# Optimization experiments

Measured on AMD Instinct MI355X. Metric: run time of the kernel, lower is better.

## Reference

```python
import jax, jax.numpy as jnp
import numpy as np

D_MODEL = 1024
N_HEADS = 16
HEAD_DIM = D_MODEL // N_HEADS
BATCH = 2
SEQ = 2048


def setup_inputs() -> dict:
    key = jax.random.key(0)
    ks = jax.random.split(key, 9)
    s = 1.0 / np.sqrt(D_MODEL)
    inp = {
        "x": jax.random.normal(ks[0], (BATCH, SEQ, D_MODEL), dtype=jnp.float32),
        "Wq": jax.random.uniform(ks[1], (D_MODEL, D_MODEL), jnp.float32, -s, s),
        "bq": jax.random.uniform(ks[2], (D_MODEL,), jnp.float32, -s, s),
        "Wk": jax.random.uniform(ks[3], (D_MODEL, D_MODEL), jnp.float32, -s, s),
        "bk": jax.random.uniform(ks[4], (D_MODEL,), jnp.float32, -s, s),
        "Wv": jax.random.uniform(ks[5], (D_MODEL, D_MODEL), jnp.float32, -s, s),
        "bv": jax.random.uniform(ks[6], (D_MODEL,), jnp.float32, -s, s),
        "Wo": jax.random.uniform(ks[7], (D_MODEL, D_MODEL), jnp.float32, -s, s),
        "bo": jax.random.uniform(ks[8], (D_MODEL,), jnp.float32, -s, s),
    }
    return inp


def reference(x, Wq, bq, Wk, bk, Wv, bv, Wo, bo):
    B, S, _ = x.shape
    # projections -> [B, H, S, Dh]
    def proj(W, b):
        y = jnp.einsum('bsd,df->bsf', x, W) + b
        return y.reshape(B, S, N_HEADS, HEAD_DIM).transpose(0, 2, 1, 3)
    q = proj(Wq, bq)
    k = proj(Wk, bk)
    v = proj(Wv, bv)
    scores = jnp.einsum('bhqd,bhkd->bhqk', q, k) / jnp.sqrt(jnp.float32(HEAD_DIM))
    mask = jnp.tril(jnp.ones((S, S), dtype=bool))  # [S, S] causal mask
    scores = jnp.where(mask, scores, -jnp.inf)
    weights = jax.nn.softmax(scores, axis=-1)
    h = jnp.einsum('bhqk,bhkd->bhqd', weights, v)
    h = h.transpose(0, 2, 1, 3).reshape(B, S, N_HEADS * HEAD_DIM)
    return jnp.einsum('bsd,df->bsf', h, Wo) + bo
```

## Files before the change

### kernel.cpp

```cpp
#include <hip/hip_runtime.h>
#include <hip/hip_bf16.h>
#include <cmath>

#define D_MODEL 1024
#define NHEADS 16
#define HDIM 64
#define BATCH 2
#define SEQ 2048
#define MROWS (BATCH*SEQ)
#define KDIM 1024

typedef unsigned short ushort_t;
typedef unsigned int uint32;
typedef __attribute__((ext_vector_type(8))) short short8;
typedef __attribute__((ext_vector_type(4))) short short4b;
typedef __attribute__((ext_vector_type(4))) float floatx4;

#define QSCALE 0.1803368801111204f
#define EXP2F(x) __builtin_amdgcn_exp2f(x)

__device__ __forceinline__ ushort_t f2bf(float x) {
    union { float f; uint32 u; } v; v.f = x;
    uint32 r = v.u + 0x7FFFu + ((v.u >> 16) & 1u);
    return (ushort_t)(r >> 16);
}

__device__ __forceinline__ uint32 pkbf(float a, float b) {
    union { __hip_bfloat162 h2; uint32 u; } v;
    v.h2 = __float22bfloat162_rn(make_float2(a, b));
    return v.u;
}

__device__ __forceinline__ void glds16(const void* g, void* l) {
    __builtin_amdgcn_global_load_lds(
        (const __attribute__((address_space(1))) void*)g,
        (__attribute__((address_space(3))) void*)l, 16, 0, 0);
}

__global__ __launch_bounds__(256)
void cvt_all(const float* __restrict__ x, const float* __restrict__ W0,
             const float* __restrict__ W1, const float* __restrict__ W2,
             const float* __restrict__ W3, ushort_t* __restrict__ xb,
             ushort_t* __restrict__ WtQKV, ushort_t* __restrict__ WtO)
{
    const int z = blockIdx.z;
    if (z == 4) {
        size_t idx = ((size_t)blockIdx.y * 32 + blockIdx.x) * 256 + threadIdx.x;
        #pragma unroll
        for (int l = 0; l < 4; ++l) {
            size_t i = ((size_t)l * 262144 + idx) * 4;
            float4 v = *(const float4*)(x + i);
            uint2 o;
            o.x = pkbf(v.x, v.y);
            o.y = pkbf(v.z, v.w);
            *(uint2*)(xb + i) = o;
        }
        return;
    }
    __shared__ float tl[32][33];
    const float* W = (z == 0) ? W0 : (z == 1) ? W1 : (z == 2) ? W2 : W3;
    ushort_t* out = (z < 3) ? (WtQKV + (size_t)z * D_MODEL * KDIM) : WtO;
    const int k0 = blockIdx.x * 32, n0 = blockIdx.y * 32;
    const int tx = threadIdx.x & 31, ty = threadIdx.x >> 5;
    #pragma unroll
    for (int i = 0; i < 4; ++i)
        tl[ty + i * 8][tx] = W[(size_t)(k0 + ty + i * 8) * D_MODEL + n0 + tx];
    __syncthreads();
    #pragma unroll
    for (int i = 0; i < 4; ++i)
        out[(size_t)(n0 + ty + i * 8) * KDIM + k0 + tx] = f2bf(tl[tx][ty + i * 8]);
}

__global__ __launch_bounds__(128, 2)
void gemm_qkv(const ushort_t* __restrict__ A, const ushort_t* __restrict__ Bt,
              const float* __restrict__ b0, const float* __restrict__ b1,
              const float* __restrict__ b2, ushort_t* __restrict__ Qb,
              ushort_t* __restrict__ Kb, ushort_t* __restrict__ Vb)
{
    __shared__ ushort_t As[128 * 64];
    __shared__ ushort_t Bs[128 * 64];

    const int tid = threadIdx.x;
    const int w = tid >> 6, lane = tid & 63;
    const int quad = lane >> 4, col = lane & 15;
    const int m0 = blockIdx.y * 128, n0 = blockIdx.x * 128;

    floatx4 zero = {0.f, 0.f, 0.f, 0.f};
    floatx4 acc[4][8];
    #pragma unroll
    for (int i = 0; i < 4; ++i)
        #pragma unroll
        for (int j = 0; j < 8; ++j) acc[i][j] = zero;

    #pragma unroll 1
    for (int k0 = 0; k0 < KDIM; k0 += 64) {
        #pragma unroll
        for (int i = 0; i < 8; ++i) {
            int c = i * 128 + tid;
            int row = c >> 3;
            int kc = (c & 7) ^ (row & 7);
            glds16(A  + (size_t)(m0 + row) * KDIM + k0 + kc * 8, As + (i * 128 + w * 64) * 8);
            glds16(Bt + (size_t)(n0 + row) * KDIM + k0 + kc * 8, Bs + (i * 128 + w * 64) * 8);
        }
        __syncthreads();
        #pragma unroll
        for (int ks = 0; ks < 2; ++ks) {
            short8 af[4], bfr[8];
            const int kc = ks * 4 + quad;
            #pragma unroll
            for (int mt = 0; mt < 4; ++mt) {
                int r = w * 64 + mt * 16 + col;
                af[mt] = *(const short8*)(As + ((size_t)r * 8 + (kc ^ (r & 7))) * 8);
            }
            #pragma unroll
            for (int nt = 0; nt < 8; ++nt) {
                int r = nt * 16 + col;
                bfr[nt] = *(const short8*)(Bs + ((size_t)r * 8 + (kc ^ (r & 7))) * 8);
            }
            #pragma unroll
            for (int mt = 0; mt < 4; ++mt)
                #pragma unroll
                for (int nt = 0; nt < 8; ++nt)
                    acc[mt][nt] = __builtin_amdgcn_mfma_f32_16x16x32_bf16(
                        af[mt], bfr[nt], acc[mt][nt], 0, 0, 0);
        }
        __syncthreads();
    }

    const int which = n0 >> 10;
    const float* bp = (which == 0) ? b0 : (which == 1) ? b1 : b2;
    if (which < 2) {
        ushort_t* outp = (which == 0) ? Qb : Kb;
        const float scl = (which == 0) ? QSCALE : 1.0f;
        #pragma unroll
        for (int mt = 0; mt < 4; ++mt)
            #pragma unroll
            for (int nt = 0; nt < 8; ++nt) {
                int nn = (n0 + nt * 16 + col) & 1023;
                float bb = bp[nn];
                int h = nn >> 6, d = nn & 63;
                #pragma unroll
                for (int r = 0; r < 4; ++r) {
                    int m = m0 + w * 64 + mt * 16 + quad * 4 + r;
                    int b = m >> 11, s = m & 2047;
                    outp[((size_t)(b * NHEADS + h) * SEQ + s) * HDIM + d] =
                        f2bf((acc[mt][nt][r] + bb) * scl);
                }
            }
    } else {
        #pragma unroll
        for (int mt = 0; mt < 4; ++mt)
            #pragma unroll
            for (int nt = 0; nt < 8; ++nt) {
                int nn = (n0 + nt * 16 + col) & 1023;
                float bb = bp[nn];
                int h = nn >> 6, d = nn & 63;
                int mb = m0 + w * 64 + mt * 16 + quad * 4;
                int b = mb >> 11, s = mb & 2047;
                uint2 pw;
                pw.x = pkbf(acc[mt][nt][0] + bb, acc[mt][nt][1] + bb);
                pw.y = pkbf(acc[mt][nt][2] + bb, acc[mt][nt][3] + bb);
                *(uint2*)(Vb + ((size_t)(b * NHEADS + h) * HDIM + d) * SEQ + s) = pw;
            }
    }
}

__global__ __launch_bounds__(128, 2)
void gemm_o(const ushort_t* __restrict__ A, const ushort_t* __restrict__ Bt,
            const float* __restrict__ b0, float* __restrict__ Cf)
{
    __shared__ ushort_t As[128 * 64];
    __shared__ ushort_t Bs[64 * 64];

    const int tid = threadIdx.x;
    const int w = tid >> 6, lane = tid & 63;
    const int quad = lane >> 4, col = lane & 15;
    const int m0 = blockIdx.y * 128, n0 = blockIdx.x * 64;

    floatx4 zero = {0.f, 0.f, 0.f, 0.f};
    floatx4 acc[4][4];
    #pragma unroll
    for (int i = 0; i < 4; ++i)
        #pragma unroll
        for (int j = 0; j < 4; ++j) acc[i][j] = zero;

    #pragma unroll 1
    for (int k0 = 0; k0 < KDIM; k0 += 64) {
        #pragma unroll
        for (int i = 0; i < 8; ++i) {
            int c = i * 128 + tid;
            int row = c >> 3;
            int kc = (c & 7) ^ (row & 7);
            glds16(A + (size_t)(m0 + row) * KDIM + k0 + kc * 8, As + (i * 128 + w * 64) * 8);
        }
        #pragma unroll
        for (int i = 0; i < 4; ++i) {
            int c = i * 128 + tid;
            int row = c >> 3;
            int kc = (c & 7) ^ (row & 7);
            glds16(Bt + (size_t)(n0 + row) * KDIM + k0 + kc * 8, Bs + (i * 128 + w * 64) * 8);
        }
        __syncthreads();
        #pragma unroll
        for (int ks = 0; ks < 2; ++ks) {
            short8 af[4], bfr[4];
            const int kc = ks * 4 + quad;
            #pragma unroll
            for (int mt = 0; mt < 4; ++mt) {
                int r = w * 64 + mt * 16 + col;
                af[mt] = *(const short8*)(As + ((size_t)r * 8 + (kc ^ (r & 7))) * 8);
            }
            #pragma unroll
            for (int nt = 0; nt < 4; ++nt) {
                int r = nt * 16 + col;
                bfr[nt] = *(const short8*)(Bs + ((size_t)r * 8 + (kc ^ (r & 7))) * 8);
            }
            #pragma unroll
            for (int mt = 0; mt < 4; ++mt)
                #pragma unroll
                for (int nt = 0; nt < 4; ++nt)
                    acc[mt][nt] = __builtin_amdgcn_mfma_f32_16x16x32_bf16(
                        af[mt], bfr[nt], acc[mt][nt], 0, 0, 0);
        }
        __syncthreads();
    }

    #pragma unroll
    for (int mt = 0; mt < 4; ++mt)
        #pragma unroll
        for (int nt = 0; nt < 4; ++nt) {
            int n = n0 + nt * 16 + col;
            float bb = b0[n];
            #pragma unroll
            for (int r = 0; r < 4; ++r) {
                int m = m0 + w * 64 + mt * 16 + quad * 4 + r;
                Cf[(size_t)m * D_MODEL + n] = acc[mt][nt][r] + bb;
            }
        }
}

__global__ __launch_bounds__(256)
void attn_mfma(const ushort_t* __restrict__ Q, const ushort_t* __restrict__ K,
               const ushort_t* __restrict__ Vt, ushort_t* __restrict__ H)
{
    __shared__ __align__(16) float smemf[16640];
    ushort_t* Qs  = (ushort_t*)smemf;
    ushort_t* Ksm = (ushort_t*)(smemf + 2048);
    ushort_t* Vsm = (ushort_t*)(smemf + 6144);
    float* Ored = smemf;
    float* Lred = smemf + 16384;

    const int tid = threadIdx.x;
    const int w = tid >> 6, lane = tid & 63;
    const int quad = lane >> 4, col = lane & 15;
    const int blk = blockIdx.x;
    const int bh = (blk & 7) * 4 + ((blk >> 3) & 3);
    const int pair = blk >> 5;
    const size_t base = (size_t)bh * SEQ * HDIM;
    const ushort_t* Kb = K + base;
    const ushort_t* Vb = Vt + base;
    const int b = bh >> 4, h = bh & 15;

    const int c0 = (w * 2 + 0) * 64 + lane;
    const int c1 = (w * 2 + 1) * 64 + lane;
    const int r0 = c0 >> 3, o0 = ((c0 & 7) ^ (r0 & 7)) * 8;
    const int r1 = c1 >> 3, o1 = ((c1 & 7) ^ (r1 & 7)) * 8;

    const int rk = w * 16 + col;
    const floatx4 zero = {0.f, 0.f, 0.f, 0.f};

    #pragma unroll 1
    for (int pi = 0; pi < 2; ++pi) {
        const int qt = pi ? pair : 31 - pair;
        const int q0 = qt * 64;
        const int nt = qt + 1;

        __syncthreads();
        #pragma unroll
        for (int i = 0; i < 2; ++i) {
            int c = (w * 2 + i) * 64 + lane;
            int row = c >> 3, kc = (c & 7) ^ (row & 7);
            glds16(Q + base + (size_t)(q0 + row) * HDIM + kc * 8, Qs + (w * 2 + i) * 512);
        }
        glds16(Kb + (size_t)r0 * HDIM + o0, Ksm + (w * 2 + 0) * 512);
        glds16(Kb + (size_t)r1 * HDIM + o1, Ksm + (w * 2 + 1) * 512);
        glds16(Vb + (size_t)r0 * SEQ + o0,  Vsm + (w * 2 + 0) * 512);
        glds16(Vb + (size_t)r1 * SEQ + o1,  Vsm + (w * 2 + 1) * 512);
        __syncthreads();

        short8 bq[4][2];
        #pragma unroll
        for (int qb = 0; qb < 4; ++qb)
            #pragma unroll
            for (int ks = 0; ks < 2; ++ks) {
                int rq = qb * 16 + col;
                int kc = ks * 4 + quad;
                bq[qb][ks] = *(const short8*)(Qs + ((size_t)rq * 8 + (kc ^ (rq & 7))) * 8);
            }

        floatx4 o_[4][4];
        #pragma unroll
        for (int i = 0; i < 4; ++i)
            #pragma unroll
            for (int j = 0; j < 4; ++j) o_[i][j] = zero;
        float lq[4] = {0.f, 0.f, 0.f, 0.f};

        #pragma unroll 1
        for (int t = 0; t < nt; ++t) {
            const ushort_t* Kcur = Ksm + (t & 1) * 4096;
            const ushort_t* Vcur = Vsm + (t & 1) * 4096;
            if (t + 1 < nt) {
                const int k0n = (t + 1) * 64;
                ushort_t* Kn = Ksm + ((t + 1) & 1) * 4096;
                ushort_t* Vn = Vsm + ((t + 1) & 1) * 4096;
                glds16(Kb + (size_t)(k0n + r0) * HDIM + o0, Kn + (w * 2 + 0) * 512);
                glds16(Kb + (size_t)(k0n + r1) * HDIM + o1, Kn + (w * 2 + 1) * 512);
                glds16(Vb + (size_t)r0 * SEQ + k0n + o0,    Vn + (w * 2 + 0) * 512);
                glds16(Vb + (size_t)r1 * SEQ + k0n + o1,    Vn + (w * 2 + 1) * 512);
            }

            floatx4 sc[4];
            #pragma unroll
            for (int qb = 0; qb < 4; ++qb) sc[qb] = zero;
            #pragma unroll
            for (int ks = 0; ks < 2; ++ks) {
                const int kc = ks * 4 + quad;
                short8 ak = *(const short8*)(Kcur + ((size_t)rk * 8 + (kc ^ (rk & 7))) * 8);
                #pragma unroll
                for (int qb = 0; qb < 4; ++qb)
                    sc[qb] = __builtin_amdgcn_mfma_f32_16x16x32_bf16(
                        ak, bq[qb][ks], sc[qb], 0, 0, 0);
            }

            if (t == nt - 1) {
                #pragma unroll
                for (int qb = 0; qb < 4; ++qb)
                    #pragma unroll
                    for (int r = 0; r < 4; ++r)
                        if (w * 16 + quad * 4 + r > qb * 16 + col) sc[qb][r] = -INFINITY;
            }

            short4b bp[4];
            #pragma unroll
            for (int qb = 0; qb < 4; ++qb) {
                float p0 = EXP2F(sc[qb][0]);
                float p1 = EXP2F(sc[qb][1]);
                float p2 = EXP2F(sc[qb][2]);
                float p3 = EXP2F(sc[qb][3]);
                lq[qb] += (p0 + p1) + (p2 + p3);
                union { uint2 u; short4b s; } pv;
                pv.u.x = pkbf(p0, p1);
                pv.u.y = pkbf(p2, p3);
                bp[qb] = pv.s;
            }

            const int cc = 2 * w + (quad >> 1);
            const int sub = (quad & 1) * 4;
            #pragma unroll
            for (int db = 0; db < 4; ++db) {
                int rv = db * 16 + col;
                short4b av = *(const short4b*)(Vcur + ((size_t)rv * 8 + (cc ^ (rv & 7))) * 8 + sub);
                #pragma unroll
                for (int qb = 0; qb < 4; ++qb)
                    o_[db][qb] = __builtin_amdgcn_mfma_f32_16x16x16bf16_1k(
                        av, bp[qb], o_[db][qb], 0, 0, 0);
            }

            __syncthreads();
        }

        #pragma unroll
        for (int qb = 0; qb < 4; ++qb) {
            lq[qb] += __shfl_xor(lq[qb], 16);
            lq[qb] += __shfl_xor(lq[qb], 32);
        }
        if (quad == 0) {
            #pragma unroll
            for (int qb = 0; qb < 4; ++qb) Lred[w * 64 + qb * 16 + col] = lq[qb];
        }
        {
            float* myreg = Ored + w * 4096;
            #pragma unroll
            for (int db = 0; db < 4; ++db)
                #pragma unroll
                for (int qb = 0; qb < 4; ++qb) {
                    int q = qb * 16 + col;
                    int swch = (db * 4 + quad) ^ col;
                    *(floatx4*)(myreg + q * 64 + swch * 4) = o_[db][qb];
                }
        }
        __syncthreads();

        {
            const int qloc = w * 16 + (lane >> 2);
            float lsum = Lred[qloc] + Lred[64 + qloc] + Lred[128 + qloc] + Lred[192 + qloc];
            float linv = 1.f / lsum;
            const int dc0 = (lane & 3) * 4;
            floatx4 acc[4];
            #pragma unroll
            for (int j = 0; j < 4; ++j) {
                int swch = (dc0 + j) ^ (qloc & 15);
                const float* p = Ored + (size_t)qloc * 64 + swch * 4;
                floatx4 a = *(const floatx4*)p;
                a += *(const floatx4*)(p + 4096);
                a += *(const floatx4*)(p + 8192);
                a += *(const floatx4*)(p + 12288);
                acc[j] = a;
            }
            const size_t rowb = ((size_t)(b * SEQ + q0 + qloc)) * D_MODEL + h * HDIM + dc0 * 4;
            uint4 u0, u1;
            u0.x = pkbf(acc[0][0] * linv, acc[0][1] * linv);
            u0.y = pkbf(acc[0][2] * linv, acc[0][3] * linv);
            u0.z = pkbf(acc[1][0] * linv, acc[1][1] * linv);
            u0.w = pkbf(acc[1][2] * linv, acc[1][3] * linv);
            u1.x = pkbf(acc[2][0] * linv, acc[2][1] * linv);
            u1.y = pkbf(acc[2][2] * linv, acc[2][3] * linv);
            u1.z = pkbf(acc[3][0] * linv, acc[3][1] * linv);
            u1.w = pkbf(acc[3][2] * linv, acc[3][3] * linv);
            *(uint4*)(H + rowb) = u0;
            *(uint4*)(H + rowb + 8) = u1;
        }
    }
}

extern "C" void kernel_launch(void* const* d_in, const int* in_sizes, int n_in,
                              void* d_out, int out_size, void* d_ws, size_t ws_size,
                              hipStream_t stream)
{
    (void)in_sizes; (void)n_in; (void)out_size; (void)ws_size;
    const float* x  = (const float*)d_in[0];
    const float* Wq = (const float*)d_in[1];
    const float* bq = (const float*)d_in[2];
    const float* Wk = (const float*)d_in[3];
    const float* bk = (const float*)d_in[4];
    const float* Wv = (const float*)d_in[5];
    const float* bv = (const float*)d_in[6];
    const float* Wo = (const float*)d_in[7];
    const float* bo = (const float*)d_in[8];

    const size_t E = (size_t)MROWS * D_MODEL;
    ushort_t* xb    = (ushort_t*)d_ws;
    ushort_t* WtQKV = xb + E;
    ushort_t* WtO   = WtQKV + 3 * (size_t)D_MODEL * KDIM;
    ushort_t* Qb    = WtO + (size_t)D_MODEL * KDIM;
    ushort_t* Kb    = Qb + E;
    ushort_t* Vb    = Kb + E;
    ushort_t* Hb    = Vb + E;

    cvt_all<<<dim3(32, 32, 5), 256, 0, stream>>>(x, Wq, Wk, Wv, Wo, xb, WtQKV, WtO);
    gemm_qkv<<<dim3(24, 32), 128, 0, stream>>>(xb, WtQKV, bq, bk, bv, Qb, Kb, Vb);
    attn_mfma<<<dim3(512), 256, 0, stream>>>(Qb, Kb, Vb, Hb);
    gemm_o<<<dim3(16, 32), 128, 0, stream>>>(Hb, WtO, bo, (float*)d_out);
}
```

Baseline: 179.2 us.

## Split attention into one query tile per block, shrink LDS, add MFMA priority

The attention kernel now launches one block per query tile (1024 blocks) instead of pairing a long and a short tile in each block. The output reduction is done in two halves over head dimension, which cuts shared memory from about 65KB to 40KB, and launch bounds request 4 blocks per CU to raise occupancy. s_setprio is raised around the MFMA sections to favour matrix issue across waves. In exchange, the causal workload is less balanced per block and Q is loaded per tile, so scheduling now depends on the hardware dispatching heavy tiles first.

Result: slower. 367.9 us (+105.3%).

```diff
diff --git a/kernel.cpp b/kernel.cpp
--- a/kernel.cpp
+++ b/kernel.cpp
@@ -239,23 +239,25 @@
         }
 }
 
-__global__ __launch_bounds__(256)
+__global__ __launch_bounds__(256, 4)
 void attn_mfma(const ushort_t* __restrict__ Q, const ushort_t* __restrict__ K,
                const ushort_t* __restrict__ Vt, ushort_t* __restrict__ H)
 {
-    __shared__ __align__(16) float smemf[16640];
+    __shared__ __align__(16) float smemf[10240];
     ushort_t* Qs  = (ushort_t*)smemf;
     ushort_t* Ksm = (ushort_t*)(smemf + 2048);
     ushort_t* Vsm = (ushort_t*)(smemf + 6144);
-    float* Ored = smemf;
-    float* Lred = smemf + 16384;
+    float* Lred = smemf;
+    float* Ored = smemf + 2048;
 
     const int tid = threadIdx.x;
     const int w = tid >> 6, lane = tid & 63;
     const int quad = lane >> 4, col = lane & 15;
     const int blk = blockIdx.x;
-    const int bh = (blk & 7) * 4 + ((blk >> 3) & 3);
-    const int pair = blk >> 5;
+    const int g5 = blk & 31;
+    const int bh = (g5 & 7) * 4 + (g5 >> 3);
+    const int grp = blk >> 5;
+    const int qt = (grp < 16) ? (31 - 2 * grp) : (2 * (grp - 16));
     const size_t base = (size_t)bh * SEQ * HDIM;
     const ushort_t* Kb = K + base;
     const ushort_t* Vb = Vt + base;
@@ -269,157 +271,164 @@
     const int rk = w * 16 + col;
     const floatx4 zero = {0.f, 0.f, 0.f, 0.f};
 
+    const int q0 = qt * 64;
+    const int nt = qt + 1;
+
+    #pragma unroll
+    for (int i = 0; i < 2; ++i) {
+        int c = (w * 2 + i) * 64 + lane;
+        int row = c >> 3, kc = (c & 7) ^ (row & 7);
+        glds16(Q + base + (size_t)(q0 + row) * HDIM + kc * 8, Qs + (w * 2 + i) * 512);
+    }
+    glds16(Kb + (size_t)r0 * HDIM + o0, Ksm + (w * 2 + 0) * 512);
+    glds16(Kb + (size_t)r1 * HDIM + o1, Ksm + (w * 2 + 1) * 512);
+    glds16(Vb + (size_t)r0 * SEQ + o0,  Vsm + (w * 2 + 0) * 512);
+    glds16(Vb + (size_t)r1 * SEQ + o1,  Vsm + (w * 2 + 1) * 512);
+    __syncthreads();
+
+    short8 bq[4][2];
+    #pragma unroll
+    for (int qb = 0; qb < 4; ++qb)
+        #pragma unroll
+        for (int ks = 0; ks < 2; ++ks) {
+            int rq = qb * 16 + col;
+            int kc = ks * 4 + quad;
+            bq[qb][ks] = *(const short8*)(Qs + ((size_t)rq * 8 + (kc ^ (rq & 7))) * 8);
+        }
+
+    floatx4 o_[4][4];
+    #pragma unroll
+    for (int i = 0; i < 4; ++i)
+        #pragma unroll
+        for (int j = 0; j < 4; ++j) o_[i][j] = zero;
+    float lq[4] = {0.f, 0.f, 0.f, 0.f};
+
     #pragma unroll 1
-    for (int pi = 0; pi < 2; ++pi) {
-        const int qt = pi ? pair : 31 - pair;
-        const int q0 = qt * 64;
-        const int nt = qt + 1;
-
-        __syncthreads();
-        #pragma unroll
-        for (int i = 0; i < 2; ++i) {
-            int c = (w * 2 + i) * 64 + lane;
-            int row = c >> 3, kc = (c & 7) ^ (row & 7);
-            glds16(Q + base + (size_t)(q0 + row) * HDIM + kc * 8, Qs + (w * 2 + i) * 512);
-        }
-        glds16(Kb + (size_t)r0 * HDIM + o0, Ksm + (w * 2 + 0) * 512);
-        glds16(Kb + (size_t)r1 * HDIM + o1, Ksm + (w * 2 + 1) * 512);
-        glds16(Vb + (size_t)r0 * SEQ + o0,  Vsm + (w * 2 + 0) * 512);
-        glds16(Vb + (size_t)r1 * SEQ + o1,  Vsm + (w * 2 + 1) * 512);
-        __syncthreads();
-
-        short8 bq[4][2];
-        #pragma unroll
-        for (int qb = 0; qb < 4; ++qb)
-            #pragma unroll
-            for (int ks = 0; ks < 2; ++ks) {
-                int rq = qb * 16 + col;
-                int kc = ks * 4 + quad;
-                bq[qb][ks] = *(const short8*)(Qs + ((size_t)rq * 8 + (kc ^ (rq & 7))) * 8);
-            }
-
-        floatx4 o_[4][4];
-        #pragma unroll
-        for (int i = 0; i < 4; ++i)
-            #pragma unroll
-            for (int j = 0; j < 4; ++j) o_[i][j] = zero;
-        float lq[4] = {0.f, 0.f, 0.f, 0.f};
-
-        #pragma unroll 1
-        for (int t = 0; t < nt; ++t) {
-            const ushort_t* Kcur = Ksm + (t & 1) * 4096;
-            const ushort_t* Vcur = Vsm + (t & 1) * 4096;
-            if (t + 1 < nt) {
-                const int k0n = (t + 1) * 64;
-                ushort_t* Kn = Ksm + ((t + 1) & 1) * 4096;
-                ushort_t* Vn = Vsm + ((t + 1) & 1) * 4096;
-                glds16(Kb + (size_t)(k0n + r0) * HDIM + o0, Kn + (w * 2 + 0) * 512);
-                glds16(Kb + (size_t)(k0n + r1) * HDIM + o1, Kn + (w * 2 + 1) * 512);
-                glds16(Vb + (size_t)r0 * SEQ + k0n + o0,    Vn + (w * 2 + 0) * 512);
-                glds16(Vb + (size_t)r1 * SEQ + k0n + o1,    Vn + (w * 2 + 1) * 512);
-            }
-
-            floatx4 sc[4];
-            #pragma unroll
-            for (int qb = 0; qb < 4; ++qb) sc[qb] = zero;
-            #pragma unroll
-            for (int ks = 0; ks < 2; ++ks) {
-                const int kc = ks * 4 + quad;
-                short8 ak = *(const short8*)(Kcur + ((size_t)rk * 8 + (kc ^ (rk & 7))) * 8);
+    for (int t = 0; t < nt; ++t) {
+        const ushort_t* Kcur = Ksm + (t & 1) * 4096;
+        const ushort_t* Vcur = Vsm + (t & 1) * 4096;
+        if (t + 1 < nt) {
+            const int k0n = (t + 1) * 64;
+            ushort_t* Kn = Ksm + ((t + 1) & 1) * 4096;
+            ushort_t* Vn = Vsm + ((t + 1) & 1) * 4096;
+            glds16(Kb + (size_t)(k0n + r0) * HDIM + o0, Kn + (w * 2 + 0) * 512);
+            glds16(Kb + (size_t)(k0n + r1) * HDIM + o1, Kn + (w * 2 + 1) * 512);
+            glds16(Vb + (size_t)r0 * SEQ + k0n + o0,    Vn + (w * 2 + 0) * 512);
+            glds16(Vb + (size_t)r1 * SEQ + k0n + o1,    Vn + (w * 2 + 1) * 512);
+        }
+
+        floatx4 sc[4];
+        #pragma unroll
+        for (int qb = 0; qb < 4; ++qb) sc[qb] = zero;
+        __builtin_amdgcn_s_setprio(1);
+        #pragma unroll
+        for (int ks = 0; ks < 2; ++ks) {
+            const int kc = ks * 4 + quad;
+            short8 ak = *(const short8*)(Kcur + ((size_t)rk * 8 + (kc ^ (rk & 7))) * 8);
+            #pragma unroll
+            for (int qb = 0; qb < 4; ++qb)
+                sc[qb] = __builtin_amdgcn_mfma_f32_16x16x32_bf16(
+                    ak, bq[qb][ks], sc[qb], 0, 0, 0);
+        }
+        __builtin_amdgcn_s_setprio(0);
+
+        if (t == nt - 1) {
+            #pragma unroll
+            for (int qb = 0; qb < 4; ++qb)
                 #pragma unroll
-                for (int qb = 0; qb < 4; ++qb)
-                    sc[qb] = __builtin_amdgcn_mfma_f32_16x16x32_bf16(
-                        ak, bq[qb][ks], sc[qb], 0, 0, 0);
-            }
-
-            if (t == nt - 1) {
-                #pragma unroll
-                for (int qb = 0; qb < 4; ++qb)
-                    #pragma unroll
-                    for (int r = 0; r < 4; ++r)
-                        if (w * 16 + quad * 4 + r > qb * 16 + col) sc[qb][r] = -INFINITY;
-            }
-
-            short4b bp[4];
-            #pragma unroll
-            for (int qb = 0; qb < 4; ++qb) {
-                float p0 = EXP2F(sc[qb][0]);
-                float p1 = EXP2F(sc[qb][1]);
-                float p2 = EXP2F(sc[qb][2]);
-                float p3 = EXP2F(sc[qb][3]);
-                lq[qb] += (p0 + p1) + (p2 + p3);
-                union { uint2 u; short4b s; } pv;
-                pv.u.x = pkbf(p0, p1);
-                pv.u.y = pkbf(p2, p3);
-                bp[qb] = pv.s;
-            }
-
-            const int cc = 2 * w + (quad >> 1);
-            const int sub = (quad & 1) * 4;
-            #pragma unroll
-            for (int db = 0; db < 4; ++db) {
-                int rv = db * 16 + col;
-                short4b av = *(const short4b*)(Vcur + ((size_t)rv * 8 + (cc ^ (rv & 7))) * 8 + sub);
-                #pragma unroll
-                for (int qb = 0; qb < 4; ++qb)
-                    o_[db][qb] = __builtin_amdgcn_mfma_f32_16x16x16bf16_1k(
-                        av, bp[qb], o_[db][qb], 0, 0, 0);
-            }
-
-            __syncthreads();
-        }
-
+                for (int r = 0; r < 4; ++r)
+                    if (w * 16 + quad * 4 + r > qb * 16 + col) sc[qb][r] = -INFINITY;
+        }
+
+        short4b bp[4];
         #pragma unroll
         for (int qb = 0; qb < 4; ++qb) {
-            lq[qb] += __shfl_xor(lq[qb], 16);
-            lq[qb] += __shfl_xor(lq[qb], 32);
-        }
-        if (quad == 0) {
-            #pragma unroll
-            for (int qb = 0; qb < 4; ++qb) Lred[w * 64 + qb * 16 + col] = lq[qb];
-        }
+            float p0 = EXP2F(sc[qb][0]);
+            float p1 = EXP2F(sc[qb][1]);
+            float p2 = EXP2F(sc[qb][2]);
+            float p3 = EXP2F(sc[qb][3]);
+            lq[qb] += (p0 + p1) + (p2 + p3);
+            union { uint2 u; short4b s; } pv;
+            pv.u.x = pkbf(p0, p1);
+            pv.u.y = pkbf(p2, p3);
+            bp[qb] = pv.s;
+        }
+
+        const int cc = 2 * w + (quad >> 1);
+        const int sub = (quad & 1) * 4;
+        __builtin_amdgcn_s_setprio(1);
+        #pragma unroll
+        for (int db = 0; db < 4; ++db) {
+            int rv = db * 16 + col;
+            short4b av = *(const short4b*)(Vcur + ((size_t)rv * 8 + (cc ^ (rv & 7))) * 8 + sub);
+            #pragma unroll
+            for (int qb = 0; qb < 4; ++qb)
+                o_[db][qb] = __builtin_amdgcn_mfma_f32_16x16x16bf16_1k(
+                    av, bp[qb], o_[db][qb], 0, 0, 0);
+        }
+        __builtin_amdgcn_s_setprio(0);
+
+        __syncthreads();
+    }
+
+    #pragma unroll
+    for (int qb = 0; qb < 4; ++qb) {
+        lq[qb] += __shfl_xor(lq[qb], 16);
+        lq[qb] += __shfl_xor(lq[qb], 32);
+    }
+    if (quad == 0) {
+        #pragma unroll
+        for (int qb = 0; qb < 4; ++qb) Lred[w * 64 + qb * 16 + col] = lq[qb];
+    }
+
+    float linv = 0.f;
+    const int lr = lane >> 2;
+    const int qloc = w * 16 + lr;
+    const int dg = lane & 3;
+    #pragma unroll 1
+    for (int p = 0; p < 2; ++p) {
         {
-            float* myreg = Ored + w * 4096;
-            #pragma unroll
-            for (int db = 0; db < 4; ++db)
+            float* myreg = Ored + w * 2048;
+            #pragma unroll
+            for (int dh = 0; dh < 2; ++dh) {
                 #pragma unroll
                 for (int qb = 0; qb < 4; ++qb) {
                     int q = qb * 16 + col;
-                    int swch = (db * 4 + quad) ^ col;
-                    *(floatx4*)(myreg + q * 64 + swch * 4) = o_[db][qb];
+                    int dc = dh * 4 + quad;
+                    int swch = dc ^ (q & 7);
+                    *(floatx4*)(myreg + q * 32 + swch * 4) = o_[p * 2 + dh][qb];
                 }
-        }
-        __syncthreads();
-
+            }
+        }
+        __syncthreads();
         {
-            const int qloc = w * 16 + (lane >> 2);
-            float lsum = Lred[qloc] + Lred[64 + qloc] + Lred[128 + qloc] + Lred[192 + qloc];
-            float linv = 1.f / lsum;
-            const int dc0 = (lane & 3) * 4;
-            floatx4 acc[4];
-            #pragma unroll
-            for (int j = 0; j < 4; ++j) {
-                int swch = (dc0 + j) ^ (qloc & 15);
-                const float* p = Ored + (size_t)qloc * 64 + swch * 4;
-                floatx4 a = *(const floatx4*)p;
-                a += *(const floatx4*)(p + 4096);
-                a += *(const floatx4*)(p + 8192);
-                a += *(const floatx4*)(p + 12288);
-                acc[j] = a;
-            }
-            const size_t rowb = ((size_t)(b * SEQ + q0 + qloc)) * D_MODEL + h * HDIM + dc0 * 4;
-            uint4 u0, u1;
-            u0.x = pkbf(acc[0][0] * linv, acc[0][1] * linv);
-            u0.y = pkbf(acc[0][2] * linv, acc[0][3] * linv);
-            u0.z = pkbf(acc[1][0] * linv, acc[1][1] * linv);
-            u0.w = pkbf(acc[1][2] * linv, acc[1][3] * linv);
-            u1.x = pkbf(acc[2][0] * linv, acc[2][1] * linv);
-            u1.y = pkbf(acc[2][2] * linv, acc[2][3] * linv);
-            u1.z = pkbf(acc[3][0] * linv, acc[3][1] * linv);
-            u1.w = pkbf(acc[3][2] * linv, acc[3][3] * linv);
-            *(uint4*)(H + rowb) = u0;
-            *(uint4*)(H + rowb + 8) = u1;
-        }
+            if (p == 0) {
+                float lsum = Lred[qloc] + Lred[64 + qloc] + Lred[128 + qloc] + Lred[192 + qloc];
+                linv = 1.f / lsum;
+            }
+            float res[8];
+            #pragma unroll
+            for (int jj = 0; jj < 2; ++jj) {
+                int j = dg * 2 + jj;
+                int swch = j ^ (lr & 7);
+                const float* pp = Ored + (size_t)qloc * 32 + swch * 4;
+                floatx4 a = *(const floatx4*)pp;
+                a += *(const floatx4*)(pp + 2048);
+                a += *(const floatx4*)(pp + 4096);
+                a += *(const floatx4*)(pp + 6144);
+                res[jj * 4 + 0] = a[0]; res[jj * 4 + 1] = a[1];
+                res[jj * 4 + 2] = a[2]; res[jj * 4 + 3] = a[3];
+            }
+            const size_t rowb = ((size_t)(b * SEQ + q0 + qloc)) * D_MODEL
+                              + h * HDIM + p * 32 + dg * 8;
+            uint4 u;
+            u.x = pkbf(res[0] * linv, res[1] * linv);
+            u.y = pkbf(res[2] * linv, res[3] * linv);
+            u.z = pkbf(res[4] * linv, res[5] * linv);
+            u.w = pkbf(res[6] * linv, res[7] * linv);
+            *(uint4*)(H + rowb) = u;
+        }
+        if (p == 0) __syncthreads();
     }
 }
 
@@ -449,6 +458,6 @@
 
     cvt_all<<<dim3(32, 32, 5), 256, 0, stream>>>(x, Wq, Wk, Wv, Wo, xb, WtQKV, WtO);
     gemm_qkv<<<dim3(24, 32), 128, 0, stream>>>(xb, WtQKV, bq, bk, bv, Qb, Kb, Vb);
-    attn_mfma<<<dim3(512), 256, 0, stream>>>(Qb, Kb, Vb, Hb);
+    attn_mfma<<<dim3(1024), 256, 0, stream>>>(Qb, Kb, Vb, Hb);
     gemm_o<<<dim3(16, 32), 128, 0, stream>>>(Hb, WtO, bo, (float*)d_out);
 }
```
